# Kernel optimization log

Measured on AMD Instinct MI355X. Metric: run time of the kernel, lower is better.

## Reference

```python
import jax, jax.numpy as jnp
import numpy as np

B, T, D = 1, 4096, 2048
H, HKV = 16, 4
DH = D // H            # 128
GROUP = H // HKV       # 4
ROPE_BASE = 10000.0


def setup_inputs() -> dict:
    key = jax.random.key(0)
    kx, kq, kk, kv, ko = jax.random.split(key, 5)
    s = 0.02
    return {
        "x": jax.random.normal(kx, (B, T, D), dtype=jnp.float32),
        "Wq": jax.random.normal(kq, (D, D), dtype=jnp.float32) * s,
        "Wk": jax.random.normal(kk, (D, HKV * DH), dtype=jnp.float32) * s,
        "Wv": jax.random.normal(kv, (D, HKV * DH), dtype=jnp.float32) * s,
        "Wo": jax.random.normal(ko, (D, D), dtype=jnp.float32) * s,
    }


def _rope_sincos(t, half):
    inv_freq = 1.0 / (ROPE_BASE ** (jnp.arange(half, dtype=jnp.float32) / half))
    ang = jnp.arange(t, dtype=jnp.float32)[:, None] * inv_freq  # [T, half]
    # broadcast over batch and head dims: [1, T, 1, half]
    return jnp.sin(ang)[None, :, None, :], jnp.cos(ang)[None, :, None, :]


def _apply_rope(x, sin, cos, half):
    x1, x2 = x[..., :half], x[..., half:]
    return jnp.concatenate([x1 * cos - x2 * sin, x1 * sin + x2 * cos], axis=-1)


def reference(x, Wq, Wk, Wv, Wo):
    b, t, d = x.shape
    q = (x @ Wq).reshape(b, t, H, DH)      # [B,T,H,Dh], H ordered (Hkv, group)
    k = (x @ Wk).reshape(b, t, HKV, DH)    # [B,T,Hkv,Dh]
    v = (x @ Wv).reshape(b, t, HKV, DH)

    half = DH // 2
    sin, cos = _rope_sincos(t, half)
    q = _apply_rope(q, sin, cos, half)
    k = _apply_rope(k, sin, cos, half)

    # GQA without materializing repeated K/V: split q heads into (kv_head, group)
    qg = q.reshape(b, t, HKV, GROUP, DH)
    att = jnp.einsum('bthgd,bshd->bhgts', qg, k) / np.float32(np.sqrt(DH))
    causal = jnp.tril(jnp.ones((t, t), dtype=bool))
    att = jnp.where(causal[None, None, None, :, :], att, -jnp.inf)
    att = jax.nn.softmax(att, axis=-1)
    y = jnp.einsum('bhgts,bshd->bthgd', att, v).reshape(b, t, d)
    return y @ Wo
```

## Files before the change

kernel.cpp:

```cpp
#include <hip/hip_runtime.h>
#include <hip/hip_bf16.h>

#define TT 4096
#define DD 2048
#define NH 16
#define NKV 4
#define DHD 128
#define NQKV 3072

typedef __attribute__((ext_vector_type(8))) short short8;
typedef __attribute__((ext_vector_type(4))) float f32x4;
typedef __hip_bfloat16 bf16;

#define GLOAD_LDS16(g, l)                                                \
    __builtin_amdgcn_global_load_lds(                                    \
        (const __attribute__((address_space(1))) unsigned int*)(g),      \
        (__attribute__((address_space(3))) unsigned int*)(l), 16, 0, 0)

__global__ void cast_x_kernel(const float* __restrict__ x, bf16* __restrict__ xb, int n) {
    int i = (blockIdx.x * blockDim.x + threadIdx.x) * 4;
    if (i >= n) return;
    float4 v = *(const float4*)(x + i);
    xb[i + 0] = __float2bfloat16(v.x);
    xb[i + 1] = __float2bfloat16(v.y);
    xb[i + 2] = __float2bfloat16(v.z);
    xb[i + 3] = __float2bfloat16(v.w);
}

__global__ void transpose_cast_all(const float* __restrict__ Wq, const float* __restrict__ Wk,
                                   const float* __restrict__ Wv, const float* __restrict__ Wo,
                                   bf16* __restrict__ Wt, bf16* __restrict__ Wot) {
    __shared__ float tile[32][33];
    const float* in;
    bf16* out;
    int N, rowOff;
    switch (blockIdx.z) {
        case 0: in = Wq; out = Wt; N = 2048; rowOff = 0; break;
        case 1: in = Wk; out = Wt; N = 512; rowOff = 2048; break;
        case 2: in = Wv; out = Wt; N = 512; rowOff = 2560; break;
        default: in = Wo; out = Wot; N = 2048; rowOff = 0; break;
    }
    int n0 = blockIdx.y * 32;
    if (n0 >= N) return;
    int k0 = blockIdx.x * 32;
    int tx = threadIdx.x, ty = threadIdx.y;
#pragma unroll
    for (int i = 0; i < 4; ++i)
        tile[ty + i * 8][tx] = in[(size_t)(k0 + ty + i * 8) * N + n0 + tx];
    __syncthreads();
#pragma unroll
    for (int i = 0; i < 4; ++i)
        out[(size_t)(rowOff + n0 + ty + i * 8) * 2048 + k0 + tx] = __float2bfloat16(tile[tx][ty + i * 8]);
}

template <bool OUT_BF16>
__global__ __launch_bounds__(256) void gemm_bt_kernel(const bf16* __restrict__ A,
                                                      const bf16* __restrict__ Bt,
                                                      void* __restrict__ C,
                                                      int M, int N, int K) {
    __shared__ bf16 As[128 * 32];
    __shared__ bf16 Bs[128 * 32];
    int nwg = gridDim.x * gridDim.y;
    int orig = blockIdx.y * gridDim.x + blockIdx.x;
    int swz = (orig & 7) * (nwg >> 3) + (orig >> 3);
    int bx = swz % gridDim.x, by = swz / gridDim.x;
    int bn0 = bx * 128, bm0 = by * 128;
    int tid = threadIdx.x;
    int wave = tid >> 6, lane = tid & 63, quad = lane >> 4, l15 = lane & 15;
    int wm = (wave >> 1) * 64, wn = (wave & 1) * 64;

    int srow = wave * 32 + (lane >> 2);
    int scol = (lane & 3) * 8;
    const bf16* gA = A + (size_t)(bm0 + srow) * K + scol;
    const bf16* gB = Bt + (size_t)(bn0 + srow) * K + scol;
    bf16* lA = As + srow * 32 + scol;
    bf16* lB = Bs + srow * 32 + scol;

    f32x4 zero = {0.f, 0.f, 0.f, 0.f};
    f32x4 acc[4][4];
#pragma unroll
    for (int i = 0; i < 4; ++i)
#pragma unroll
        for (int j = 0; j < 4; ++j) acc[i][j] = zero;

    for (int k0 = 0; k0 < K; k0 += 32) {
        GLOAD_LDS16(gA + k0, lA);
        GLOAD_LDS16(gA + k0 + (size_t)16 * K, lA + 16 * 32);
        GLOAD_LDS16(gB + k0, lB);
        GLOAD_LDS16(gB + k0 + (size_t)16 * K, lB + 16 * 32);
        __syncthreads();
        short8 af[4], bfr[4];
#pragma unroll
        for (int i = 0; i < 4; ++i) af[i] = *(const short8*)&As[(wm + i * 16 + l15) * 32 + quad * 8];
#pragma unroll
        for (int j = 0; j < 4; ++j) bfr[j] = *(const short8*)&Bs[(wn + j * 16 + l15) * 32 + quad * 8];
#pragma unroll
        for (int i = 0; i < 4; ++i)
#pragma unroll
            for (int j = 0; j < 4; ++j)
                acc[i][j] = __builtin_amdgcn_mfma_f32_16x16x32_bf16(af[i], bfr[j], acc[i][j], 0, 0, 0);
        __syncthreads();
    }
#pragma unroll
    for (int i = 0; i < 4; ++i)
#pragma unroll
        for (int j = 0; j < 4; ++j)
#pragma unroll
            for (int r = 0; r < 4; ++r) {
                int row = bm0 + wm + i * 16 + quad * 4 + r;
                int col = bn0 + wn + j * 16 + l15;
                float v = acc[i][j][r];
                if (OUT_BF16)
                    ((bf16*)C)[(size_t)row * N + col] = __float2bfloat16(v);
                else
                    ((float*)C)[(size_t)row * N + col] = v;
            }
}

__global__ void rope_split_kernel(const bf16* __restrict__ QKV, bf16* __restrict__ Qs,
                                  bf16* __restrict__ Ks, bf16* __restrict__ Vt) {
    int slot = blockIdx.x * 4 + (threadIdx.x >> 6);
    int d = threadIdx.x & 63;
    int t = slot / 24, c = slot % 24;
    const bf16* base = QKV + (size_t)t * NQKV;
    int off = (c < 16) ? c * 128 : (c < 20) ? 2048 + (c - 16) * 128 : 2560 + (c - 20) * 128;
    float x1 = __bfloat162float(base[off + d]);
    float x2 = __bfloat162float(base[off + 64 + d]);
    float o1, o2;
    if (c < 20) {
        float invf = __expf((float)d * -0.14391156831f);
        float ang = (float)t * invf;
        float sn = sinf(ang), cs = cosf(ang);
        o1 = x1 * cs - x2 * sn;
        o2 = x1 * sn + x2 * cs;
    } else {
        o1 = x1;
        o2 = x2;
    }
    if (c < 16) {
        const float scale = 0.12751741f;
        o1 *= scale;
        o2 *= scale;
        bf16* dst = Qs + ((size_t)c * TT + t) * DHD;
        dst[d] = __float2bfloat16(o1);
        dst[d + 64] = __float2bfloat16(o2);
    } else if (c < 20) {
        bf16* dst = Ks + ((size_t)(c - 16) * TT + t) * DHD;
        dst[d] = __float2bfloat16(o1);
        dst[d + 64] = __float2bfloat16(o2);
    } else {
        int gg = c - 20;
        Vt[((size_t)gg * DHD + d) * TT + t] = __float2bfloat16(o1);
        Vt[((size_t)gg * DHD + d + 64) * TT + t] = __float2bfloat16(o2);
    }
}

__global__ __launch_bounds__(512) __attribute__((amdgpu_waves_per_eu(4, 4)))
void attn_kernel(const bf16* __restrict__ Qs,
                 const bf16* __restrict__ Ks,
                 const bf16* __restrict__ Vt,
                 bf16* __restrict__ Y) {
    __shared__ char smem[81920];
    int h = blockIdx.y, bpair = blockIdx.x, g = h >> 2;
    int tid = threadIdx.x, wave = tid >> 6, lane = tid & 63, quad = lane >> 4, l15 = lane & 15;
    int grp = wave >> 2;
    int w = wave & 3;
    int gtid = tid & 255;

    bf16* KsL = (bf16*)(smem + grp * 32768);
    bf16* VtL = (bf16*)(smem + grp * 32768 + 16384);
    bf16* PsW = (bf16*)(smem + 65536) + wave * (16 * 64);
    float* Obuf = (float*)(smem + 32768);
    float* mlbuf = (float*)(smem + 80896);

    const bf16* kg = Ks + (size_t)g * TT * DHD;
    const bf16* vg = Vt + (size_t)g * DHD * TT;
    f32x4 zero = {0.f, 0.f, 0.f, 0.f};

    int koffl[4], voffl[4], ldsl[4];
#pragma unroll
    for (int r = 0; r < 4; ++r) {
        int idx = r * 256 + gtid;
        int krow = idx >> 4, kch = (idx & 15) ^ (krow & 15);
        koffl[r] = krow * DHD + kch * 8;
        int vrow = idx >> 3, vch = (idx & 7) ^ (vrow & 7);
        voffl[r] = vrow * TT + vch * 8;
        ldsl[r] = idx * 8;
    }

    for (int pass = 0; pass < 2; ++pass) {
        int qt = (pass == 0) ? bpair : 63 - bpair;
        int qbase = qt * 64 + w * 16;

        short8 qf[4];
        const bf16* qptr = Qs + ((size_t)h * TT + qbase + l15) * DHD + quad * 8;
#pragma unroll
        for (int ks = 0; ks < 4; ++ks) qf[ks] = *(const short8*)(qptr + ks * 32);

        f32x4 acc[8];
#pragma unroll
        for (int i = 0; i < 8; ++i) acc[i] = zero;
        float m_i = -1e30f, l_i = 0.f;

        const bf16* kSrc = kg + (size_t)grp * 64 * DHD;
        const bf16* vSrc = vg + grp * 64;
        int nIter = (qt >> 1) + 1;
        for (int it = 0; it < nIter; ++it) {
            int kt = it * 2 + grp;
            bool active = (kt <= qt);
            bool diag = (kt == qt);
            __syncthreads();
            if (active) {
#pragma unroll
                for (int r = 0; r < 4; ++r) {
                    GLOAD_LDS16(kSrc + koffl[r], KsL + ldsl[r]);
                    GLOAD_LDS16(vSrc + voffl[r], VtL + ldsl[r]);
                }
            }
            kSrc += 128 * DHD;
            vSrc += 128;
            __syncthreads();

            if (active) {
                f32x4 s[4];
                __builtin_amdgcn_s_setprio(1);
#pragma unroll
                for (int nt = 0; nt < 4; ++nt) {
                    if (!diag || nt <= w) {
                        s[nt] = zero;
#pragma unroll
                        for (int ks = 0; ks < 4; ++ks) {
                            int ch = (ks * 4 + quad) ^ l15;
                            short8 kf = *(const short8*)&KsL[(nt * 16 + l15) * 128 + ch * 8];
                            s[nt] = __builtin_amdgcn_mfma_f32_16x16x32_bf16(kf, qf[ks], s[nt], 0, 0, 0);
                        }
                        if (diag && nt == w) {
#pragma unroll
                            for (int r = 0; r < 4; ++r)
                                if (quad * 4 + r > l15) s[nt][r] = -1e30f;
                        }
                    } else {
#pragma unroll
                        for (int r = 0; r < 4; ++r) s[nt][r] = -1e30f;
                    }
                }
                __builtin_amdgcn_s_setprio(0);

                float mloc = -1e30f;
#pragma unroll
                for (int nt = 0; nt < 4; ++nt)
#pragma unroll
                    for (int r = 0; r < 4; ++r) mloc = fmaxf(mloc, s[nt][r]);
                mloc = fmaxf(mloc, __shfl_xor(mloc, 16));
                mloc = fmaxf(mloc, __shfl_xor(mloc, 32));
                float mnew = fmaxf(m_i, mloc);
                bool up = __any(mloc > m_i);
                float alpha = up ? exp2f(m_i - mnew) : 1.0f;
                float sl = 0.f;
#pragma unroll
                for (int nt = 0; nt < 4; ++nt)
#pragma unroll
                    for (int r = 0; r < 4; ++r) {
                        s[nt][r] = exp2f(s[nt][r] - mnew);
                        sl += s[nt][r];
                    }
                sl += __shfl_xor(sl, 16);
                sl += __shfl_xor(sl, 32);
                l_i = l_i * alpha + sl;
                m_i = mnew;
                if (up) {
#pragma unroll
                    for (int d8 = 0; d8 < 8; ++d8)
#pragma unroll
                        for (int r = 0; r < 4; ++r) acc[d8][r] *= alpha;
                }

#pragma unroll
                for (int nt = 0; nt < 4; ++nt)
#pragma unroll
                    for (int rr = 0; rr < 2; ++rr) {
                        int col = nt * 16 + quad * 4 + rr * 2;
                        int ch = (col >> 3) ^ (l15 & 7);
                        __hip_bfloat162 pk;
                        pk.x = __float2bfloat16(s[nt][rr * 2]);
                        pk.y = __float2bfloat16(s[nt][rr * 2 + 1]);
                        *(__hip_bfloat162*)&PsW[l15 * 64 + ch * 8 + (col & 7)] = pk;
                    }
                asm volatile("s_waitcnt lgkmcnt(0)" ::: "memory");

                int kkmax = diag ? (w >> 1) + 1 : 2;
                __builtin_amdgcn_s_setprio(1);
#pragma unroll
                for (int kk = 0; kk < 2; ++kk) {
                    if (kk < kkmax) {
                        int chp = (kk * 4 + quad) ^ (l15 & 7);
                        short8 pf = *(const short8*)&PsW[l15 * 64 + chp * 8];
#pragma unroll
                        for (int d8 = 0; d8 < 8; ++d8) {
                            short8 vf = *(const short8*)&VtL[(d8 * 16 + l15) * 64 + chp * 8];
                            acc[d8] = __builtin_amdgcn_mfma_f32_16x16x32_bf16(vf, pf, acc[d8], 0, 0, 0);
                        }
                    }
                }
                __builtin_amdgcn_s_setprio(0);
            }
        }

        __syncthreads();
        if (quad == 0) {
            mlbuf[(wave * 16 + l15) * 2] = m_i;
            mlbuf[(wave * 16 + l15) * 2 + 1] = l_i;
        }
        __syncthreads();
        if (grp == 1) {
            float m_a = mlbuf[(w * 16 + l15) * 2];
            float mm = fmaxf(m_a, m_i);
            float fb = exp2f(m_i - mm);
            float* ob = Obuf + (w * 16 + l15) * 132;
#pragma unroll
            for (int d8 = 0; d8 < 8; ++d8) {
                f32x4 t = acc[d8] * fb;
                *(f32x4*)&ob[d8 * 16 + quad * 4] = t;
            }
        }
        __syncthreads();
        if (grp == 0) {
            float m_b = mlbuf[((w + 4) * 16 + l15) * 2];
            float l_b = mlbuf[((w + 4) * 16 + l15) * 2 + 1];
            float mm = fmaxf(m_i, m_b);
            float fa = exp2f(m_i - mm);
            float fb = exp2f(m_b - mm);
            float lt = l_i * fa + l_b * fb;
            float* ob = Obuf + (w * 16 + l15) * 132;
#pragma unroll
            for (int d8 = 0; d8 < 8; ++d8) {
                f32x4 t = *(const f32x4*)&ob[d8 * 16 + quad * 4];
                acc[d8] = acc[d8] * fa + t;
            }
            float linv = 1.0f / lt;

            bf16* ow = (bf16*)smem + w * 2048;
#pragma unroll
            for (int d8 = 0; d8 < 8; ++d8)
#pragma unroll
                for (int rr = 0; rr < 2; ++rr) {
                    int colD = d8 * 16 + quad * 4 + rr * 2;
                    int ch = (colD >> 3) ^ (l15 & 7);
                    __hip_bfloat162 o2;
                    o2.x = __float2bfloat16(acc[d8][rr * 2] * linv);
                    o2.y = __float2bfloat16(acc[d8][rr * 2 + 1] * linv);
                    *(__hip_bfloat162*)&ow[l15 * 128 + ch * 8 + (colD & 7)] = o2;
                }
            asm volatile("s_waitcnt lgkmcnt(0)" ::: "memory");
#pragma unroll
            for (int c = 0; c < 4; ++c) {
                int chunk = quad * 4 + c;
                int ch = chunk ^ (l15 & 7);
                short8 ov = *(const short8*)&ow[l15 * 128 + ch * 8];
                *(short8*)&Y[(size_t)(qbase + l15) * DD + h * DHD + chunk * 8] = ov;
            }
        }
        __syncthreads();
    }
}

extern "C" void kernel_launch(void* const* d_in, const int* in_sizes, int n_in,
                              void* d_out, int out_size, void* d_ws, size_t ws_size,
                              hipStream_t stream) {
    const float* x = (const float*)d_in[0];
    const float* Wq = (const float*)d_in[1];
    const float* Wk = (const float*)d_in[2];
    const float* Wv = (const float*)d_in[3];
    const float* Wo = (const float*)d_in[4];

    char* ws = (char*)d_ws;
    size_t off = 0;
    auto alloc = [&](size_t bytes) {
        void* p = ws + off;
        off += (bytes + 255) & ~(size_t)255;
        return p;
    };
    bf16* xb = (bf16*)alloc((size_t)TT * DD * 2);
    bf16* Wt = (bf16*)alloc((size_t)NQKV * DD * 2);
    bf16* Wot = (bf16*)alloc((size_t)DD * DD * 2);
    bf16* QKVb = (bf16*)alloc((size_t)TT * NQKV * 2);
    bf16* Qs = (bf16*)alloc((size_t)NH * TT * DHD * 2);
    bf16* Ksb = (bf16*)alloc((size_t)NKV * TT * DHD * 2);
    bf16* Vtb = (bf16*)alloc((size_t)NKV * DHD * TT * 2);
    bf16* Yb = (bf16*)alloc((size_t)TT * DD * 2);

    cast_x_kernel<<<(TT * DD / 4 + 255) / 256, 256, 0, stream>>>(x, xb, TT * DD);
    transpose_cast_all<<<dim3(64, 64, 4), dim3(32, 8), 0, stream>>>(Wq, Wk, Wv, Wo, Wt, Wot);

    gemm_bt_kernel<true><<<dim3(NQKV / 128, TT / 128), 256, 0, stream>>>(xb, Wt, QKVb, TT, NQKV, DD);
    rope_split_kernel<<<TT * 24 / 4, 256, 0, stream>>>(QKVb, Qs, Ksb, Vtb);
    attn_kernel<<<dim3(32, NH), 512, 0, stream>>>(Qs, Ksb, Vtb, Yb);
    gemm_bt_kernel<false><<<dim3(DD / 128, TT / 128), 256, 0, stream>>>(Yb, Wot, d_out, TT, DD, DD);
}
```

Before: 400.7 us.

## Double-buffer K/V tiles in attention and add a separate V transpose kernel

The attention kernel now uses 32-key tiles per wave group with a double-buffered LDS ring. The next tile's K/V global-to-LDS loads are issued before computing on the current one, so load latency can overlap with compute and one barrier per iteration is removed. The tile split changes the causal-skip logic to a per-wave diagonal offset, and LDS shrinks to allow a launch bound of 4 blocks. The rope kernel now writes V row-major, and a new tiled transpose kernel produces the transposed V, replacing scattered strided stores at the cost of an extra launch and buffer.

```diff
diff --git a/kernel.cpp b/kernel.cpp
--- a/kernel.cpp
+++ b/kernel.cpp
@@ -118,7 +118,7 @@
 }
 
 __global__ void rope_split_kernel(const bf16* __restrict__ QKV, bf16* __restrict__ Qs,
-                                  bf16* __restrict__ Ks, bf16* __restrict__ Vt) {
+                                  bf16* __restrict__ Ks, bf16* __restrict__ Vr) {
     int slot = blockIdx.x * 4 + (threadIdx.x >> 6);
     int d = threadIdx.x & 63;
     int t = slot / 24, c = slot % 24;
@@ -150,43 +150,66 @@
         dst[d + 64] = __float2bfloat16(o2);
     } else {
         int gg = c - 20;
-        Vt[((size_t)gg * DHD + d) * TT + t] = __float2bfloat16(o1);
-        Vt[((size_t)gg * DHD + d + 64) * TT + t] = __float2bfloat16(o2);
-    }
-}
-
-__global__ __launch_bounds__(512) __attribute__((amdgpu_waves_per_eu(4, 4)))
-void attn_kernel(const bf16* __restrict__ Qs,
-                 const bf16* __restrict__ Ks,
-                 const bf16* __restrict__ Vt,
-                 bf16* __restrict__ Y) {
-    __shared__ char smem[81920];
+        bf16* dst = Vr + ((size_t)gg * TT + t) * DHD;
+        dst[d] = __float2bfloat16(o1);
+        dst[d + 64] = __float2bfloat16(o2);
+    }
+}
+
+__global__ void transpose_v_kernel(const bf16* __restrict__ Vr, bf16* __restrict__ Vt) {
+    __shared__ short tile[64][80];
+    int g = blockIdx.z;
+    int t0 = blockIdx.x * 64, d0 = blockIdx.y * 64;
+    int tid = threadIdx.x;
+#pragma unroll
+    for (int i = 0; i < 2; ++i) {
+        int lin = i * 2048 + tid * 8;
+        int r = lin >> 6, c = lin & 63;
+        *(short8*)&tile[r][c] = *(const short8*)(Vr + ((size_t)g * TT + t0 + r) * DHD + d0 + c);
+    }
+    __syncthreads();
+#pragma unroll
+    for (int i = 0; i < 2; ++i) {
+        int lin = i * 2048 + tid * 8;
+        int r = lin >> 6, c = lin & 63;
+        short8 v;
+#pragma unroll
+        for (int j = 0; j < 8; ++j) v[j] = tile[c + j][r];
+        *(short8*)(Vt + ((size_t)g * DHD + d0 + r) * TT + t0 + c) = v;
+    }
+}
+
+__global__ __launch_bounds__(512, 4) void attn_kernel(const bf16* __restrict__ Qs,
+                                                      const bf16* __restrict__ Ks,
+                                                      const bf16* __restrict__ Vt,
+                                                      bf16* __restrict__ Y) {
+    __shared__ __attribute__((aligned(16))) char smem[74752];
     int h = blockIdx.y, bpair = blockIdx.x, g = h >> 2;
     int tid = threadIdx.x, wave = tid >> 6, lane = tid & 63, quad = lane >> 4, l15 = lane & 15;
     int grp = wave >> 2;
     int w = wave & 3;
     int gtid = tid & 255;
 
-    bf16* KsL = (bf16*)(smem + grp * 32768);
-    bf16* VtL = (bf16*)(smem + grp * 32768 + 16384);
-    bf16* PsW = (bf16*)(smem + 65536) + wave * (16 * 64);
+    char* Kbase = smem + grp * 32768;
+    bf16* PsW = (bf16*)(smem + 65536 + wave * 1024);
     float* Obuf = (float*)(smem + 32768);
-    float* mlbuf = (float*)(smem + 80896);
+    float* mlbuf = (float*)(smem + 73728);
 
     const bf16* kg = Ks + (size_t)g * TT * DHD;
     const bf16* vg = Vt + (size_t)g * DHD * TT;
     f32x4 zero = {0.f, 0.f, 0.f, 0.f};
 
-    int koffl[4], voffl[4], ldsl[4];
-#pragma unroll
-    for (int r = 0; r < 4; ++r) {
+    int kOff[2], vOff[2], lOff[2];
+#pragma unroll
+    for (int r = 0; r < 2; ++r) {
         int idx = r * 256 + gtid;
-        int krow = idx >> 4, kch = (idx & 15) ^ (krow & 15);
-        koffl[r] = krow * DHD + kch * 8;
-        int vrow = idx >> 3, vch = (idx & 7) ^ (vrow & 7);
-        voffl[r] = vrow * TT + vch * 8;
-        ldsl[r] = idx * 8;
-    }
+        int krow = idx >> 4;
+        kOff[r] = krow * DHD + ((idx & 15) ^ (krow & 15)) * 8;
+        int vrow = idx >> 2;
+        vOff[r] = vrow * TT + ((idx & 3) ^ ((vrow >> 1) & 3)) * 8;
+        lOff[r] = idx * 8;
+    }
+    int fsw = (l15 >> 1) & 3;
 
     for (int pass = 0; pass < 2; ++pass) {
         int qt = (pass == 0) ? bpair : 63 - bpair;
@@ -202,39 +225,45 @@
         for (int i = 0; i < 8; ++i) acc[i] = zero;
         float m_i = -1e30f, l_i = 0.f;
 
-        const bf16* kSrc = kg + (size_t)grp * 64 * DHD;
-        const bf16* vSrc = vg + grp * 64;
-        int nIter = (qt >> 1) + 1;
-        for (int it = 0; it < nIter; ++it) {
-            int kt = it * 2 + grp;
-            bool active = (kt <= qt);
-            bool diag = (kt == qt);
-            __syncthreads();
-            if (active) {
-#pragma unroll
-                for (int r = 0; r < 4; ++r) {
-                    GLOAD_LDS16(kSrc + koffl[r], KsL + ldsl[r]);
-                    GLOAD_LDS16(vSrc + voffl[r], VtL + ldsl[r]);
+        const bf16* kS = kg + (size_t)(grp * 32) * DHD;
+        const bf16* vS = vg + grp * 32;
+        int nIter = qt + 1;
+
+#pragma unroll
+        for (int r = 0; r < 2; ++r) {
+            GLOAD_LDS16(kS + kOff[r], (bf16*)Kbase + lOff[r]);
+            GLOAD_LDS16(vS + vOff[r], (bf16*)(Kbase + 16384) + lOff[r]);
+        }
+        __syncthreads();
+
+        int boff = 0;
+        for (int j = 0; j < nIter; ++j) {
+            int kt = 2 * j + grp;
+            if (j + 1 < nIter) {
+#pragma unroll
+                for (int r = 0; r < 2; ++r) {
+                    GLOAD_LDS16(kS + 64 * DHD + kOff[r], (bf16*)(Kbase + (boff ^ 8192)) + lOff[r]);
+                    GLOAD_LDS16(vS + 64 + vOff[r], (bf16*)(Kbase + 16384 + (boff ^ 8192)) + lOff[r]);
                 }
             }
-            kSrc += 128 * DHD;
-            vSrc += 128;
-            __syncthreads();
-
-            if (active) {
-                f32x4 s[4];
+            const bf16* Kl = (const bf16*)(Kbase + boff);
+            const bf16* Vl = (const bf16*)(Kbase + 16384 + boff);
+            int dbase = 2 * kt - 4 * qt - w;
+            if (dbase <= 0) {
+                f32x4 s[2];
                 __builtin_amdgcn_s_setprio(1);
 #pragma unroll
-                for (int nt = 0; nt < 4; ++nt) {
-                    if (!diag || nt <= w) {
+                for (int nt = 0; nt < 2; ++nt) {
+                    int dnt = dbase + nt;
+                    if (dnt <= 0) {
                         s[nt] = zero;
 #pragma unroll
                         for (int ks = 0; ks < 4; ++ks) {
                             int ch = (ks * 4 + quad) ^ l15;
-                            short8 kf = *(const short8*)&KsL[(nt * 16 + l15) * 128 + ch * 8];
+                            short8 kf = *(const short8*)&Kl[(nt * 16 + l15) * 128 + ch * 8];
                             s[nt] = __builtin_amdgcn_mfma_f32_16x16x32_bf16(kf, qf[ks], s[nt], 0, 0, 0);
                         }
-                        if (diag && nt == w) {
+                        if (dnt == 0) {
 #pragma unroll
                             for (int r = 0; r < 4; ++r)
                                 if (quad * 4 + r > l15) s[nt][r] = -1e30f;
@@ -248,7 +277,7 @@
 
                 float mloc = -1e30f;
 #pragma unroll
-                for (int nt = 0; nt < 4; ++nt)
+                for (int nt = 0; nt < 2; ++nt)
 #pragma unroll
                     for (int r = 0; r < 4; ++r) mloc = fmaxf(mloc, s[nt][r]);
                 mloc = fmaxf(mloc, __shfl_xor(mloc, 16));
@@ -258,7 +287,7 @@
                 float alpha = up ? exp2f(m_i - mnew) : 1.0f;
                 float sl = 0.f;
 #pragma unroll
-                for (int nt = 0; nt < 4; ++nt)
+                for (int nt = 0; nt < 2; ++nt)
 #pragma unroll
                     for (int r = 0; r < 4; ++r) {
                         s[nt][r] = exp2f(s[nt][r] - mnew);
@@ -276,37 +305,34 @@
                 }
 
 #pragma unroll
-                for (int nt = 0; nt < 4; ++nt)
+                for (int nt = 0; nt < 2; ++nt)
 #pragma unroll
                     for (int rr = 0; rr < 2; ++rr) {
                         int col = nt * 16 + quad * 4 + rr * 2;
-                        int ch = (col >> 3) ^ (l15 & 7);
+                        int ch = (col >> 3) ^ fsw;
                         __hip_bfloat162 pk;
                         pk.x = __float2bfloat16(s[nt][rr * 2]);
                         pk.y = __float2bfloat16(s[nt][rr * 2 + 1]);
-                        *(__hip_bfloat162*)&PsW[l15 * 64 + ch * 8 + (col & 7)] = pk;
+                        *(__hip_bfloat162*)&PsW[l15 * 32 + ch * 8 + (col & 7)] = pk;
                     }
                 asm volatile("s_waitcnt lgkmcnt(0)" ::: "memory");
 
-                int kkmax = diag ? (w >> 1) + 1 : 2;
+                int chp = quad ^ fsw;
+                short8 pf = *(const short8*)&PsW[l15 * 32 + chp * 8];
                 __builtin_amdgcn_s_setprio(1);
 #pragma unroll
-                for (int kk = 0; kk < 2; ++kk) {
-                    if (kk < kkmax) {
-                        int chp = (kk * 4 + quad) ^ (l15 & 7);
-                        short8 pf = *(const short8*)&PsW[l15 * 64 + chp * 8];
-#pragma unroll
-                        for (int d8 = 0; d8 < 8; ++d8) {
-                            short8 vf = *(const short8*)&VtL[(d8 * 16 + l15) * 64 + chp * 8];
-                            acc[d8] = __builtin_amdgcn_mfma_f32_16x16x32_bf16(vf, pf, acc[d8], 0, 0, 0);
-                        }
-                    }
+                for (int d8 = 0; d8 < 8; ++d8) {
+                    short8 vf = *(const short8*)&Vl[(d8 * 16 + l15) * 32 + chp * 8];
+                    acc[d8] = __builtin_amdgcn_mfma_f32_16x16x32_bf16(vf, pf, acc[d8], 0, 0, 0);
                 }
                 __builtin_amdgcn_s_setprio(0);
             }
+            __syncthreads();
+            boff ^= 8192;
+            kS += 64 * DHD;
+            vS += 64;
         }
 
-        __syncthreads();
         if (quad == 0) {
             mlbuf[(wave * 16 + l15) * 2] = m_i;
             mlbuf[(wave * 16 + l15) * 2 + 1] = l_i;
@@ -386,6 +412,7 @@
     bf16* QKVb = (bf16*)alloc((size_t)TT * NQKV * 2);
     bf16* Qs = (bf16*)alloc((size_t)NH * TT * DHD * 2);
     bf16* Ksb = (bf16*)alloc((size_t)NKV * TT * DHD * 2);
+    bf16* Vrb = (bf16*)alloc((size_t)NKV * TT * DHD * 2);
     bf16* Vtb = (bf16*)alloc((size_t)NKV * DHD * TT * 2);
     bf16* Yb = (bf16*)alloc((size_t)TT * DD * 2);
 
@@ -393,7 +420,8 @@
     transpose_cast_all<<<dim3(64, 64, 4), dim3(32, 8), 0, stream>>>(Wq, Wk, Wv, Wo, Wt, Wot);
 
     gemm_bt_kernel<true><<<dim3(NQKV / 128, TT / 128), 256, 0, stream>>>(xb, Wt, QKVb, TT, NQKV, DD);
-    rope_split_kernel<<<TT * 24 / 4, 256, 0, stream>>>(QKVb, Qs, Ksb, Vtb);
+    rope_split_kernel<<<TT * 24 / 4, 256, 0, stream>>>(QKVb, Qs, Ksb, Vrb);
+    transpose_v_kernel<<<dim3(TT / 64, DHD / 64, NKV), 256, 0, stream>>>(Vrb, Vtb);
     attn_kernel<<<dim3(32, NH), 512, 0, stream>>>(Qs, Ksb, Vtb, Yb);
     gemm_bt_kernel<false><<<dim3(DD / 128, TT / 128), 256, 0, stream>>>(Yb, Wot, d_out, TT, DD, DD);
 }
```

New measurement: 394.9 us. Within noise of the previous version (-1.4%).
